# Kernel tuning notes

Measured on AMD Instinct MI355X. Metric: run time of the kernel, lower is better.

Reference implementation:

```python
import jax, jax.numpy as jnp
import numpy as np

N, C, T = 64, 128, 2048
S = 9          # shift_size
D = 1          # dilation
EPS = 1e-5


def setup_inputs() -> dict:
    key = jax.random.key(0)
    k1, k2 = jax.random.split(key)
    x = jax.random.normal(k1, (N, C, T), dtype=jnp.float32)
    conv_w = jax.random.normal(k2, (C, S), dtype=jnp.float32) * (1.0 / np.sqrt(S))
    gamma = jnp.ones((C,), dtype=jnp.float32)
    beta = jnp.zeros((C,), dtype=jnp.float32)
    return {"x": x, "conv_w": conv_w, "gamma": gamma, "beta": beta}


def reference(x, conv_w, gamma, beta):
    n, c, t = x.shape
    s = conv_w.shape[1]
    # --- per-channel temporal shift with zero fill (vectorized shift()) ---
    sh = ((jnp.arange(c) % s) - s // 2) * D                    # [C]
    idx = jnp.arange(t)[None, :] - sh[:, None]                 # [C, T] source index
    valid = (idx >= 0) & (idx < t)
    idxc = jnp.clip(idx, 0, t - 1)
    xs = jnp.take_along_axis(x, jnp.broadcast_to(idxc[None], (n, c, t)), axis=2)
    xs = jnp.where(valid[None], xs, 0.0)                       # [N, C, T]
    # --- zero-pad channel dim then unfold windows of size S, stride 1 (q=1) ---
    pad_top = s // 2
    pad_bot = s // 2 - (1 if s % 2 == 0 else 0)
    xp = jnp.pad(xs, ((0, 0), (pad_top, pad_bot), (0, 0)))     # [N, C+pads, T]
    win_idx = jnp.arange(c)[:, None] + jnp.arange(s)[None, :]  # [C, S]
    w = xp[:, win_idx, :]                                      # [N, C, S, T]
    # --- grouped 1x1 conv: each output channel i mixes its S-window ---
    out = jnp.einsum('ncst,cs->nct', w, conv_w)                # [N, C, T]
    # --- BatchNorm1d (training-mode batch stats, biased var) + ReLU ---
    mean = out.mean(axis=(0, 2), keepdims=True)
    var = ((out - mean) ** 2).mean(axis=(0, 2), keepdims=True)
    out = (out - mean) * jax.lax.rsqrt(var + EPS)
    out = out * gamma[None, :, None] + beta[None, :, None]
    return jax.nn.relu(out)
```

## Files before the change

kernel.cpp:

```cpp
#include <hip/hip_runtime.h>

#define NN 64
#define CC 128
#define TT 2048
#define SS 9
#define PAD 4
#define EPSF 1e-5f
#define TL 32
#define ROWS (CC + 2 * PAD)
#define STRIDE 36
#define NB 16

__device__ __forceinline__ void stage_tile(
    const float* __restrict__ xn, float* __restrict__ ls,
    const int t0, const int tid)
{
    const bool interior = (t0 != 0) && (t0 != TT - TL);
#pragma unroll
    for (int p = 0; p < 5; ++p) {
        const int f = tid + 256 * p;
        const int r = f >> 3;
        if (r < ROWS) {
            const int j0 = (f & 7) * 4;
            const int c2 = r - PAD;
            float4 v = make_float4(0.f, 0.f, 0.f, 0.f);
            if (c2 >= 0 && c2 < CC) {
                const int sh = c2 % SS - PAD;
                const int t  = t0 + j0 - sh;
                const float* __restrict__ row = xn + (size_t)c2 * TT;
                if (interior) {
                    __builtin_memcpy(&v, row + t, sizeof(float4));
                } else {
                    v.x = (t     >= 0 && t     < TT) ? row[t]     : 0.f;
                    v.y = (t + 1 >= 0 && t + 1 < TT) ? row[t + 1] : 0.f;
                    v.z = (t + 2 >= 0 && t + 2 < TT) ? row[t + 2] : 0.f;
                    v.w = (t + 3 >= 0 && t + 3 < TT) ? row[t + 3] : 0.f;
                }
            }
            *reinterpret_cast<float4*>(&ls[r * STRIDE + j0]) = v;
        }
    }
}

__global__ __launch_bounds__(256, 8) void conv_stats(
    const float* __restrict__ x, const float* __restrict__ cw,
    float* __restrict__ buckets)
{
    __shared__ float ls[ROWS * STRIDE];

    const int n   = blockIdx.y;
    const int t0  = blockIdx.x * TL;
    const int tid = threadIdx.x;
    const float* __restrict__ xn = x + (size_t)n * CC * TT;

    stage_tile(xn, ls, t0, tid);

    const int c  = tid & (CC - 1);
    const int jb = (tid >> 7) * (TL / 2);
    float wv[SS];
#pragma unroll
    for (int s = 0; s < SS; ++s) wv[s] = cw[c * SS + s];

    __syncthreads();

    const int base = c * STRIDE + jb;
    float res[TL / 2];
#pragma unroll
    for (int j = 0; j < TL / 2; ++j) res[j] = 0.f;
#pragma unroll
    for (int s = 0; s < SS; ++s) {
        const float4* rp = reinterpret_cast<const float4*>(&ls[base + s * STRIDE]);
        float4 r0 = rp[0], r1 = rp[1], r2 = rp[2], r3 = rp[3];
        const float w = wv[s];
        res[0]  = fmaf(w, r0.x, res[0]);  res[1]  = fmaf(w, r0.y, res[1]);
        res[2]  = fmaf(w, r0.z, res[2]);  res[3]  = fmaf(w, r0.w, res[3]);
        res[4]  = fmaf(w, r1.x, res[4]);  res[5]  = fmaf(w, r1.y, res[5]);
        res[6]  = fmaf(w, r1.z, res[6]);  res[7]  = fmaf(w, r1.w, res[7]);
        res[8]  = fmaf(w, r2.x, res[8]);  res[9]  = fmaf(w, r2.y, res[9]);
        res[10] = fmaf(w, r2.z, res[10]); res[11] = fmaf(w, r2.w, res[11]);
        res[12] = fmaf(w, r3.x, res[12]); res[13] = fmaf(w, r3.y, res[13]);
        res[14] = fmaf(w, r3.z, res[14]); res[15] = fmaf(w, r3.w, res[15]);
    }
    float s1 = 0.f, s2 = 0.f;
#pragma unroll
    for (int j = 0; j < TL / 2; ++j) {
        s1 += res[j];
        s2 = fmaf(res[j], res[j], s2);
    }

    __syncthreads();
    ls[tid]       = s1;
    ls[256 + tid] = s2;
    __syncthreads();
    if (tid < CC) {
        float* bs = buckets + ((blockIdx.x + blockIdx.y) & (NB - 1)) * 2 * CC;
        atomicAdd(&bs[tid],      ls[tid]       + ls[tid + 128]);
        atomicAdd(&bs[CC + tid], ls[256 + tid] + ls[256 + tid + 128]);
    }
}

__global__ __launch_bounds__(256, 8) void conv_norm_store(
    const float* __restrict__ x, const float* __restrict__ cw,
    const float* __restrict__ buckets, const float* __restrict__ gamma,
    const float* __restrict__ beta, float* __restrict__ out)
{
    __shared__ float ls[ROWS * STRIDE];

    const int n   = blockIdx.y;
    const int t0  = blockIdx.x * TL;
    const int tid = threadIdx.x;
    const float* __restrict__ xn = x + (size_t)n * CC * TT;

    const int c  = tid & (CC - 1);
    const int jb = (tid >> 7) * (TL / 2);

    float t1 = 0.f, t2 = 0.f;
#pragma unroll
    for (int k = 0; k < NB; ++k) {
        t1 += buckets[k * 2 * CC + c];
        t2 += buckets[k * 2 * CC + CC + c];
    }
    const float inv_cnt = 1.0f / (float)(NN * TT);
    const float mean = t1 * inv_cnt;
    const float var  = t2 * inv_cnt - mean * mean;
    const float inv  = rsqrtf(var + EPSF);
    const float g = gamma[c] * inv;
    const float b = beta[c] - mean * g;

    float wv[SS];
#pragma unroll
    for (int s = 0; s < SS; ++s) wv[s] = cw[c * SS + s];

    stage_tile(xn, ls, t0, tid);
    __syncthreads();

    const int base = c * STRIDE + jb;
    float res[TL / 2];
#pragma unroll
    for (int j = 0; j < TL / 2; ++j) res[j] = 0.f;
#pragma unroll
    for (int s = 0; s < SS; ++s) {
        const float4* rp = reinterpret_cast<const float4*>(&ls[base + s * STRIDE]);
        float4 r0 = rp[0], r1 = rp[1], r2 = rp[2], r3 = rp[3];
        const float w = wv[s];
        res[0]  = fmaf(w, r0.x, res[0]);  res[1]  = fmaf(w, r0.y, res[1]);
        res[2]  = fmaf(w, r0.z, res[2]);  res[3]  = fmaf(w, r0.w, res[3]);
        res[4]  = fmaf(w, r1.x, res[4]);  res[5]  = fmaf(w, r1.y, res[5]);
        res[6]  = fmaf(w, r1.z, res[6]);  res[7]  = fmaf(w, r1.w, res[7]);
        res[8]  = fmaf(w, r2.x, res[8]);  res[9]  = fmaf(w, r2.y, res[9]);
        res[10] = fmaf(w, r2.z, res[10]); res[11] = fmaf(w, r2.w, res[11]);
        res[12] = fmaf(w, r3.x, res[12]); res[13] = fmaf(w, r3.y, res[13]);
        res[14] = fmaf(w, r3.z, res[14]); res[15] = fmaf(w, r3.w, res[15]);
    }
    __syncthreads();

#pragma unroll
    for (int q = 0; q < 4; ++q) {
        float4 v;
        v.x = fmaf(res[4 * q],     g, b);
        v.y = fmaf(res[4 * q + 1], g, b);
        v.z = fmaf(res[4 * q + 2], g, b);
        v.w = fmaf(res[4 * q + 3], g, b);
        v.x = v.x > 0.f ? v.x : 0.f;
        v.y = v.y > 0.f ? v.y : 0.f;
        v.z = v.z > 0.f ? v.z : 0.f;
        v.w = v.w > 0.f ? v.w : 0.f;
        *reinterpret_cast<float4*>(&ls[c * STRIDE + jb + 4 * q]) = v;
    }
    __syncthreads();

    float* __restrict__ on = out + (size_t)n * CC * TT + t0;
#pragma unroll
    for (int k = 0; k < 4; ++k) {
        const int f   = tid + 256 * k;
        const int row = f >> 3;
        const int q   = (f & 7) * 4;
        const float4 v = *reinterpret_cast<const float4*>(&ls[row * STRIDE + q]);
        *reinterpret_cast<float4*>(on + (size_t)row * TT + q) = v;
    }
}

extern "C" void kernel_launch(void* const* d_in, const int* in_sizes, int n_in,
                              void* d_out, int out_size, void* d_ws, size_t ws_size,
                              hipStream_t stream)
{
    const float* x     = (const float*)d_in[0];
    const float* cw    = (const float*)d_in[1];
    const float* gamma = (const float*)d_in[2];
    const float* beta  = (const float*)d_in[3];
    float* out     = (float*)d_out;
    float* buckets = (float*)d_ws;

    hipMemsetAsync(buckets, 0, (size_t)NB * 2 * CC * sizeof(float), stream);

    dim3 grid(TT / TL, NN);
    conv_stats<<<grid, 256, 0, stream>>>(x, cw, buckets);
    conv_norm_store<<<grid, 256, 0, stream>>>(x, cw, buckets, gamma, beta, out);
}
```

Baseline: 147.5 us.

## Process two time tiles per block with register prefetch of second tile

Each block now handles two consecutive 32-wide time tiles. The second tile's global loads are issued into registers before the first tile's convolution, then written to shared memory afterward, overlapping memory latency with compute. The grid halves and launch bounds drop to 4 blocks per CU to accommodate the extra registers, trading occupancy for explicit prefetch and fewer blocks/atomics.

```diff
diff --git a/kernel.cpp b/kernel.cpp
--- a/kernel.cpp
+++ b/kernel.cpp
@@ -7,66 +7,58 @@
 #define PAD 4
 #define EPSF 1e-5f
 #define TL 32
+#define TPB 64
 #define ROWS (CC + 2 * PAD)
 #define STRIDE 36
 #define NB 16
 
-__device__ __forceinline__ void stage_tile(
-    const float* __restrict__ xn, float* __restrict__ ls,
-    const int t0, const int tid)
-{
-    const bool interior = (t0 != 0) && (t0 != TT - TL);
+__device__ __forceinline__ void tile_load(
+    const float* __restrict__ xn, const int tb, const int tid,
+    const bool interior, float4 (&v)[5])
+{
 #pragma unroll
     for (int p = 0; p < 5; ++p) {
         const int f = tid + 256 * p;
         const int r = f >> 3;
+        v[p] = make_float4(0.f, 0.f, 0.f, 0.f);
         if (r < ROWS) {
-            const int j0 = (f & 7) * 4;
             const int c2 = r - PAD;
-            float4 v = make_float4(0.f, 0.f, 0.f, 0.f);
             if (c2 >= 0 && c2 < CC) {
+                const int j0 = (f & 7) * 4;
                 const int sh = c2 % SS - PAD;
-                const int t  = t0 + j0 - sh;
+                const int t  = tb + j0 - sh;
                 const float* __restrict__ row = xn + (size_t)c2 * TT;
                 if (interior) {
-                    __builtin_memcpy(&v, row + t, sizeof(float4));
+                    __builtin_memcpy(&v[p], row + t, sizeof(float4));
                 } else {
-                    v.x = (t     >= 0 && t     < TT) ? row[t]     : 0.f;
-                    v.y = (t + 1 >= 0 && t + 1 < TT) ? row[t + 1] : 0.f;
-                    v.z = (t + 2 >= 0 && t + 2 < TT) ? row[t + 2] : 0.f;
-                    v.w = (t + 3 >= 0 && t + 3 < TT) ? row[t + 3] : 0.f;
+                    v[p].x = (t     >= 0 && t     < TT) ? row[t]     : 0.f;
+                    v[p].y = (t + 1 >= 0 && t + 1 < TT) ? row[t + 1] : 0.f;
+                    v[p].z = (t + 2 >= 0 && t + 2 < TT) ? row[t + 2] : 0.f;
+                    v[p].w = (t + 3 >= 0 && t + 3 < TT) ? row[t + 3] : 0.f;
                 }
             }
-            *reinterpret_cast<float4*>(&ls[r * STRIDE + j0]) = v;
-        }
-    }
-}
-
-__global__ __launch_bounds__(256, 8) void conv_stats(
-    const float* __restrict__ x, const float* __restrict__ cw,
-    float* __restrict__ buckets)
-{
-    __shared__ float ls[ROWS * STRIDE];
-
-    const int n   = blockIdx.y;
-    const int t0  = blockIdx.x * TL;
-    const int tid = threadIdx.x;
-    const float* __restrict__ xn = x + (size_t)n * CC * TT;
-
-    stage_tile(xn, ls, t0, tid);
-
-    const int c  = tid & (CC - 1);
-    const int jb = (tid >> 7) * (TL / 2);
-    float wv[SS];
-#pragma unroll
-    for (int s = 0; s < SS; ++s) wv[s] = cw[c * SS + s];
-
-    __syncthreads();
-
-    const int base = c * STRIDE + jb;
-    float res[TL / 2];
-#pragma unroll
-    for (int j = 0; j < TL / 2; ++j) res[j] = 0.f;
+        }
+    }
+}
+
+__device__ __forceinline__ void tile_write(
+    float* __restrict__ ls, const int tid, const float4 (&v)[5])
+{
+#pragma unroll
+    for (int p = 0; p < 5; ++p) {
+        const int f = tid + 256 * p;
+        const int r = f >> 3;
+        if (r < ROWS)
+            *reinterpret_cast<float4*>(&ls[r * STRIDE + (f & 7) * 4]) = v[p];
+    }
+}
+
+__device__ __forceinline__ void conv_tile(
+    const float* __restrict__ ls, const int base, const float (&wv)[SS],
+    float (&res)[16])
+{
+#pragma unroll
+    for (int j = 0; j < 16; ++j) res[j] = 0.f;
 #pragma unroll
     for (int s = 0; s < SS; ++s) {
         const float4* rp = reinterpret_cast<const float4*>(&ls[base + s * STRIDE]);
@@ -81,12 +73,49 @@
         res[12] = fmaf(w, r3.x, res[12]); res[13] = fmaf(w, r3.y, res[13]);
         res[14] = fmaf(w, r3.z, res[14]); res[15] = fmaf(w, r3.w, res[15]);
     }
+}
+
+__global__ __launch_bounds__(256, 4) void conv_stats(
+    const float* __restrict__ x, const float* __restrict__ cw,
+    float* __restrict__ buckets)
+{
+    __shared__ float ls[ROWS * STRIDE];
+
+    const int n   = blockIdx.y;
+    const int tA  = blockIdx.x * TPB;
+    const int tB  = tA + TL;
+    const int tid = threadIdx.x;
+    const float* __restrict__ xn = x + (size_t)n * CC * TT;
+
+    float4 va[5];
+    tile_load(xn, tA, tid, blockIdx.x != 0, va);
+    tile_write(ls, tid, va);
+
+    const int c  = tid & (CC - 1);
+    const int jb = (tid >> 7) * (TL / 2);
+    float wv[SS];
+#pragma unroll
+    for (int s = 0; s < SS; ++s) wv[s] = cw[c * SS + s];
+
+    __syncthreads();
+
+    float4 vb[5];
+    tile_load(xn, tB, tid, (int)blockIdx.x != (int)gridDim.x - 1, vb);
+
+    const int base = c * STRIDE + jb;
+    float res[16];
+    conv_tile(ls, base, wv, res);
     float s1 = 0.f, s2 = 0.f;
 #pragma unroll
-    for (int j = 0; j < TL / 2; ++j) {
-        s1 += res[j];
-        s2 = fmaf(res[j], res[j], s2);
-    }
+    for (int j = 0; j < 16; ++j) { s1 += res[j]; s2 = fmaf(res[j], res[j], s2); }
+
+    __syncthreads();
+    tile_write(ls, tid, vb);
+    __syncthreads();
+
+    conv_tile(ls, base, wv, res);
+#pragma unroll
+    for (int j = 0; j < 16; ++j) { s1 += res[j]; s2 = fmaf(res[j], res[j], s2); }
 
     __syncthreads();
     ls[tid]       = s1;
@@ -99,7 +128,7 @@
     }
 }
 
-__global__ __launch_bounds__(256, 8) void conv_norm_store(
+__global__ __launch_bounds__(256, 4) void conv_norm_store(
     const float* __restrict__ x, const float* __restrict__ cw,
     const float* __restrict__ buckets, const float* __restrict__ gamma,
     const float* __restrict__ beta, float* __restrict__ out)
@@ -107,7 +136,8 @@
     __shared__ float ls[ROWS * STRIDE];
 
     const int n   = blockIdx.y;
-    const int t0  = blockIdx.x * TL;
+    const int tA  = blockIdx.x * TPB;
+    const int tB  = tA + TL;
     const int tid = threadIdx.x;
     const float* __restrict__ xn = x + (size_t)n * CC * TT;
 
@@ -127,56 +157,59 @@
     const float g = gamma[c] * inv;
     const float b = beta[c] - mean * g;
 
+    float4 va[5];
+    tile_load(xn, tA, tid, blockIdx.x != 0, va);
+    tile_write(ls, tid, va);
+
     float wv[SS];
 #pragma unroll
     for (int s = 0; s < SS; ++s) wv[s] = cw[c * SS + s];
 
-    stage_tile(xn, ls, t0, tid);
-    __syncthreads();
+    __syncthreads();
+
+    float4 vb[5];
+    tile_load(xn, tB, tid, (int)blockIdx.x != (int)gridDim.x - 1, vb);
 
     const int base = c * STRIDE + jb;
-    float res[TL / 2];
-#pragma unroll
-    for (int j = 0; j < TL / 2; ++j) res[j] = 0.f;
-#pragma unroll
-    for (int s = 0; s < SS; ++s) {
-        const float4* rp = reinterpret_cast<const float4*>(&ls[base + s * STRIDE]);
-        float4 r0 = rp[0], r1 = rp[1], r2 = rp[2], r3 = rp[3];
-        const float w = wv[s];
-        res[0]  = fmaf(w, r0.x, res[0]);  res[1]  = fmaf(w, r0.y, res[1]);
-        res[2]  = fmaf(w, r0.z, res[2]);  res[3]  = fmaf(w, r0.w, res[3]);
-        res[4]  = fmaf(w, r1.x, res[4]);  res[5]  = fmaf(w, r1.y, res[5]);
-        res[6]  = fmaf(w, r1.z, res[6]);  res[7]  = fmaf(w, r1.w, res[7]);
-        res[8]  = fmaf(w, r2.x, res[8]);  res[9]  = fmaf(w, r2.y, res[9]);
-        res[10] = fmaf(w, r2.z, res[10]); res[11] = fmaf(w, r2.w, res[11]);
-        res[12] = fmaf(w, r3.x, res[12]); res[13] = fmaf(w, r3.y, res[13]);
-        res[14] = fmaf(w, r3.z, res[14]); res[15] = fmaf(w, r3.w, res[15]);
-    }
-    __syncthreads();
-
-#pragma unroll
-    for (int q = 0; q < 4; ++q) {
-        float4 v;
-        v.x = fmaf(res[4 * q],     g, b);
-        v.y = fmaf(res[4 * q + 1], g, b);
-        v.z = fmaf(res[4 * q + 2], g, b);
-        v.w = fmaf(res[4 * q + 3], g, b);
-        v.x = v.x > 0.f ? v.x : 0.f;
-        v.y = v.y > 0.f ? v.y : 0.f;
-        v.z = v.z > 0.f ? v.z : 0.f;
-        v.w = v.w > 0.f ? v.w : 0.f;
-        *reinterpret_cast<float4*>(&ls[c * STRIDE + jb + 4 * q]) = v;
-    }
-    __syncthreads();
-
-    float* __restrict__ on = out + (size_t)n * CC * TT + t0;
-#pragma unroll
-    for (int k = 0; k < 4; ++k) {
-        const int f   = tid + 256 * k;
-        const int row = f >> 3;
-        const int q   = (f & 7) * 4;
-        const float4 v = *reinterpret_cast<const float4*>(&ls[row * STRIDE + q]);
-        *reinterpret_cast<float4*>(on + (size_t)row * TT + q) = v;
+    float res[16];
+
+#pragma unroll
+    for (int half = 0; half < 2; ++half) {
+        conv_tile(ls, base, wv, res);
+        __syncthreads();
+
+#pragma unroll
+        for (int q = 0; q < 4; ++q) {
+            float4 v;
+            v.x = fmaf(res[4 * q],     g, b);
+            v.y = fmaf(res[4 * q + 1], g, b);
+            v.z = fmaf(res[4 * q + 2], g, b);
+            v.w = fmaf(res[4 * q + 3], g, b);
+            v.x = v.x > 0.f ? v.x : 0.f;
+            v.y = v.y > 0.f ? v.y : 0.f;
+            v.z = v.z > 0.f ? v.z : 0.f;
+            v.w = v.w > 0.f ? v.w : 0.f;
+            *reinterpret_cast<float4*>(&ls[c * STRIDE + jb + 4 * q]) = v;
+        }
+        __syncthreads();
+
+        float* __restrict__ on = out + (size_t)n * CC * TT
+                               + (half == 0 ? tA : tB);
+#pragma unroll
+        for (int k = 0; k < 4; ++k) {
+            const int f   = tid + 256 * k;
+            const int row = f >> 3;
+            const int q   = (f & 7) * 4;
+            const float4 v =
+                *reinterpret_cast<const float4*>(&ls[row * STRIDE + q]);
+            *reinterpret_cast<float4*>(on + (size_t)row * TT + q) = v;
+        }
+
+        if (half == 0) {
+            __syncthreads();
+            tile_write(ls, tid, vb);
+            __syncthreads();
+        }
     }
 }
 
@@ -193,7 +226,7 @@
 
     hipMemsetAsync(buckets, 0, (size_t)NB * 2 * CC * sizeof(float), stream);
 
-    dim3 grid(TT / TL, NN);
+    dim3 grid(TT / TPB, NN);
     conv_stats<<<grid, 256, 0, stream>>>(x, cw, buckets);
     conv_norm_store<<<grid, 256, 0, stream>>>(x, cw, buckets, gamma, beta, out);
 }
```

Measured after the change: 141.7 us. -3.9%, faster.
